# Kernel optimization log

Measured on AMD Instinct MI355X. Metric: run time of the kernel, lower is better.

## Reference

```python
import jax, jax.numpy as jnp
import numpy as np

SEQ_LEN = 2048
EMBED = 1024
HIDDEN = 1024
BATCH = 4


def setup_inputs() -> dict:
    key = jax.random.key(0)
    ks = jax.random.split(key, 7)
    # xavier_uniform for weights: limit = sqrt(6/(fan_in+fan_out))
    lim = float(np.sqrt(6.0 / (EMBED + HIDDEN)))
    blim = float(1.0 / np.sqrt(EMBED))  # torch Linear default bias init U(-1/sqrt(fan_in), ...)
    inputs = jax.random.normal(ks[0], (BATCH, SEQ_LEN, EMBED), dtype=jnp.float32)
    Wq = jax.random.uniform(ks[1], (HIDDEN, EMBED), jnp.float32, -lim, lim)
    Wk = jax.random.uniform(ks[2], (HIDDEN, EMBED), jnp.float32, -lim, lim)
    Wv = jax.random.uniform(ks[3], (HIDDEN, EMBED), jnp.float32, -lim, lim)
    bq = jax.random.uniform(ks[4], (HIDDEN,), jnp.float32, -blim, blim)
    bk = jax.random.uniform(ks[5], (HIDDEN,), jnp.float32, -blim, blim)
    bv = jax.random.uniform(ks[6], (HIDDEN,), jnp.float32, -blim, blim)
    return {"inputs": inputs, "Wq": Wq, "bq": bq, "Wk": Wk, "bk": bk, "Wv": Wv, "bv": bv}


def reference(inputs, Wq, bq, Wk, bk, Wv, bv):
    B, S, E = inputs.shape
    q = jnp.einsum('bse,he->bsh', inputs, Wq) + bq  # [B,S,H]
    k = jnp.einsum('bse,he->bsh', inputs, Wk) + bk
    v = jnp.einsum('bse,he->bsh', inputs, Wv) + bv
    # NOTE: source scales by 1/sqrt(embed_size), not hidden_size
    scores = jnp.einsum('bqh,bkh->bqk', q, k) / jnp.sqrt(jnp.float32(E))
    causal = jnp.tril(jnp.ones((S, S), dtype=bool))  # [S,S]
    scores = jnp.where(causal[None, :, :], scores, -jnp.inf)
    attn = jax.nn.softmax(scores, axis=-1)
    return jnp.einsum('bqk,bkh->bqh', attn, v)
```

## Files before the change

kernel.cpp:

```cpp
#include <hip/hip_runtime.h>
#include <cstdint>
#include <cstddef>
#include <math.h>

typedef unsigned short u16;

#define S_LEN 2048
#define EMB   1024
#define HID   1024
#define NB    4

using bf16x8 = __attribute__((ext_vector_type(8))) __bf16;
using f32x4  = __attribute__((ext_vector_type(4))) float;


__device__ __forceinline__ u16 f2bf(float f) {
  union { float f; uint32_t u; } c; c.f = f;
  uint32_t u = c.u;
  uint32_t r = (u + 0x7fffu + ((u >> 16) & 1u)) >> 16;
  return (u16)r;
}

__device__ __forceinline__ float bf2f(uint32_t hi16) {
  union { uint32_t u; float f; } c; c.u = hi16;
  return c.f;
}

__device__ __forceinline__ void gld_lds16(const u16* g, u16* l) {
  auto gp = (const __attribute__((address_space(1))) uint32_t*)(uintptr_t)(const void*)g;
  auto lp = (__attribute__((address_space(3))) uint32_t*)(uintptr_t)(void*)l;
  __builtin_amdgcn_global_load_lds(gp, lp, 16, 0, 0);
}


__global__ void cvt_all(const float* __restrict__ x,  const float* __restrict__ wq,
                        const float* __restrict__ wk, const float* __restrict__ wv,
                        u16* __restrict__ xb, u16* __restrict__ wb, int nx4, int nw4lg2) {
  const int nw4 = 1 << nw4lg2;
  const int total = nx4 + 3 * nw4;
  int i = blockIdx.x * blockDim.x + threadIdx.x;
  const int stride = gridDim.x * blockDim.x;
  for (; i < total; i += stride) {
    const float* src; u16* dst; int j;
    if (i < nx4) { src = x; dst = xb; j = i; }
    else {
      const int k = i - nx4;
      const int wsel = k >> nw4lg2;
      j = k & (nw4 - 1);
      src = (wsel == 0) ? wq : (wsel == 1) ? wk : wv;
      dst = wb + ((size_t)wsel << (nw4lg2 + 2));
    }
    float4 v = reinterpret_cast<const float4*>(src)[j];
    reinterpret_cast<ushort4*>(dst)[j] =
      make_ushort4(f2bf(v.x), f2bf(v.y), f2bf(v.z), f2bf(v.w));
  }
}


template<int EPI>
__global__ __launch_bounds__(256, 2)
void gemmT(const u16* __restrict__ A, const u16* __restrict__ Bw, void* __restrict__ Cv,
           const float* __restrict__ b0, const float* __restrict__ b1,
           const float* __restrict__ b2, u16* __restrict__ VT,
           int N, long sA, long sB, long sC, float scale)
{
  constexpr int K = 1024;
  constexpr int NTILE = K / 64;
  const int z = blockIdx.z;
  A  += (long)z * sA;
  Bw += (long)z * sB;

  __shared__ __align__(16) u16 smem[32768];

  const int tid = threadIdx.x;
  const int l   = tid & 63;
  const int w   = tid >> 6;
  const int wr  = w >> 1;
  const int wc  = w & 1;

  int bm, bn;
  if constexpr (EPI == 2) {
    const int x0 = blockIdx.x;
    const int x  = (x0 & 7) * ((int)gridDim.x >> 3) + (x0 >> 3);
    int bi = (int)((sqrtf(8.0f * (float)x + 1.0f) - 1.0f) * 0.5f);
    while ((bi + 1) * (bi + 2) / 2 <= x) ++bi;
    while (bi * (bi + 1) / 2 > x) --bi;
    bm = bi * 128;
    bn = (x - bi * (bi + 1) / 2) * 128;
  } else {
    const int nwg = gridDim.x * gridDim.y;
    const int lin = blockIdx.y * gridDim.x + blockIdx.x;
    const int sw  = (lin & 7) * (nwg >> 3) + (lin >> 3);
    bm = (sw / gridDim.x) * 128;
    bn = (sw % gridDim.x) * 128;
  }

  const int arow = w * 16 + (l >> 2);
  const int acs  = (l & 3) ^ (((l >> 5) & 1) << 1);
  const u16* gbA  = A  + (long)(bm + arow) * K + acs * 8;
  const u16* gbA2 = gbA + 64L * K;
  const u16* gbB  = Bw + (long)(bn + arow) * K + acs * 8;
  const u16* gbB2 = gbB + 64L * K;

#define STGH(t, s, dbase)                                                       \
  do {                                                                          \
    const long _o = (long)(t) * 64 + (s) * 32;                                  \
    gld_lds16(gbA  + _o, smem + (dbase) + (s) * 4096 +        w * 512);         \
    gld_lds16(gbA2 + _o, smem + (dbase) + (s) * 4096 + 2048 + w * 512);         \
    gld_lds16(gbB  + _o, smem + (dbase) + 8192 + (s) * 4096 +        w * 512);  \
    gld_lds16(gbB2 + _o, smem + (dbase) + 8192 + (s) * 4096 + 2048 + w * 512);  \
  } while (0)

  const int lr  = l & 15;
  const int kg  = l >> 4;
  const int kgp = kg ^ (((lr >> 3) & 1) << 1);
  int aoff[4], boff[4];
#pragma unroll
  for (int m = 0; m < 4; ++m) aoff[m] = (wr * 64 + m * 16 + lr) * 32 + kgp * 8;
#pragma unroll
  for (int n = 0; n < 4; ++n) boff[n] = (wc * 64 + n * 16 + lr) * 32 + kgp * 8;

  f32x4 acc[4][4] = {};

  STGH(0, 0, 0);
  STGH(0, 1, 0);
  asm volatile("s_waitcnt vmcnt(0)" ::: "memory");
  __builtin_amdgcn_s_barrier();
  asm volatile("" ::: "memory");

#define PHASE(d, s, STGSTMT)                                                    \
  do {                                                                          \
    const u16* hA = smem + (d) * 16384 + (s) * 4096;                            \
    const u16* hB = smem + (d) * 16384 + 8192 + (s) * 4096;                     \
    bf16x8 av[4], bv[4];                                                        \
    _Pragma("unroll")                                                           \
    for (int m_ = 0; m_ < 4; ++m_)                                              \
      av[m_] = *reinterpret_cast<const bf16x8*>(hA + aoff[m_]);                 \
    _Pragma("unroll")                                                           \
    for (int n_ = 0; n_ < 4; ++n_)                                              \
      bv[n_] = *reinterpret_cast<const bf16x8*>(hB + boff[n_]);                 \
    STGSTMT;                                                                    \
    asm volatile("s_waitcnt vmcnt(4)" ::: "memory");                            \
    __builtin_amdgcn_s_barrier();                                               \
    asm volatile("" ::: "memory");                                              \
    __builtin_amdgcn_s_setprio(1);                                              \
    _Pragma("unroll")                                                           \
    for (int m_ = 0; m_ < 4; ++m_)                                              \
      _Pragma("unroll")                                                         \
      for (int n_ = 0; n_ < 4; ++n_)                                            \
        acc[m_][n_] = __builtin_amdgcn_mfma_f32_16x16x32_bf16(                  \
            av[m_], bv[n_], acc[m_][n_], 0, 0, 0);                              \
    __builtin_amdgcn_s_setprio(0);                                              \
    asm volatile("" ::: "memory");                                              \
  } while (0)

#pragma unroll 1
  for (int i = 0; i < NTILE / 2; ++i) {
    const int t1 = 2 * i + 1;
    const int t2 = (2 * i + 2 < NTILE) ? 2 * i + 2 : NTILE - 1;
    PHASE(0, 0, STGH(t1, 0, 16384));
    PHASE(0, 1, STGH(t1, 1, 16384));
    PHASE(1, 0, STGH(t2, 0, 0));
    PHASE(1, 1, STGH(t2, 1, 0));
  }
#undef PHASE
#undef STGH

  if constexpr (EPI == 2) {
    u16* C = (u16*)Cv + (long)z * sC;
#pragma unroll
    for (int n = 0; n < 4; ++n) {
      const int col = bn + wc * 64 + n * 16 + lr;
#pragma unroll
      for (int m = 0; m < 4; ++m) {
        const int row0 = bm + wr * 64 + m * 16 + kg * 4;
#pragma unroll
        for (int q = 0; q < 4; ++q) {
          const int row = row0 + q;
          float v = acc[m][n][q] * scale;
          if (col > row) v = -1e30f;
          C[(long)row * N + col] = f2bf(v);
        }
      }
    }
  } else {
    constexpr long M = (long)NB * S_LEN;
    const int sel = bn >> 10;
    const float* bias = (sel == 0) ? b0 : (sel == 1) ? b1 : b2;
    u16* QK = (u16*)Cv;
#pragma unroll
    for (int n = 0; n < 4; ++n) {
      const int col = bn + wc * 64 + n * 16 + lr;
      const int h   = col & (HID - 1);
      const float bbv = bias[h];
#pragma unroll
      for (int m = 0; m < 4; ++m) {
        const int row0 = bm + wr * 64 + m * 16 + kg * 4;
        if (sel < 2) {
          u16* dst = QK + (long)sel * M * HID + (long)row0 * HID + h;
#pragma unroll
          for (int q = 0; q < 4; ++q)
            dst[(long)q * HID] = f2bf(acc[m][n][q] + bbv);
        } else {
          const int b = row0 >> 11;
          const int s = row0 & (S_LEN - 1);
          ushort4 o = make_ushort4(f2bf(acc[m][n][0] + bbv), f2bf(acc[m][n][1] + bbv),
                                   f2bf(acc[m][n][2] + bbv), f2bf(acc[m][n][3] + bbv));
          *reinterpret_cast<ushort4*>(VT + ((long)b * HID + h) * S_LEN + s) = o;
        }
      }
    }
  }
}


__global__ __launch_bounds__(512, 2)
void gemm_pv(const u16* __restrict__ Pm, const u16* __restrict__ VTm, float* __restrict__ Cm)
{
  const int z = blockIdx.z;
  const u16* A = Pm  + (long)z * S_LEN * S_LEN;
  const u16* B = VTm + (long)z * HID * S_LEN;
  float*    Cz = Cm  + (long)z * S_LEN * HID;

  __shared__ __align__(16) u16 smem[32768];

  const int tid = threadIdx.x;
  const int l   = tid & 63;
  const int w   = tid >> 6;
  const int wr  = w >> 2;
  const int wc  = w & 3;
  const int bn  = blockIdx.x * 128;
  const int pr  = blockIdx.y;

  const int lr  = l & 15;
  const int kg  = l >> 4;
  const int kgp = kg ^ (((lr >> 3) & 1) << 1);
  int aoff[4], boff[2];
#pragma unroll
  for (int m = 0; m < 4; ++m) aoff[m] = (wr * 64 + m * 16 + lr) * 32 + kgp * 8;
#pragma unroll
  for (int n = 0; n < 2; ++n) boff[n] = (wc * 32 + n * 16 + lr) * 32 + kgp * 8;

  const int arow = w * 16 + (l >> 2);
  const int acs  = (l & 3) ^ (((l >> 5) & 1) << 1);

#pragma unroll 1
  for (int it = 0; it < 2; ++it) {
    const int bi = (it == 0) ? (15 - pr) : pr;
    const int bm = bi * 128;
    const int NTILE = (bi + 1) * 2;

    const u16* gbA = A + (long)(bm + arow) * S_LEN + acs * 8;
    const u16* gbB = B + (long)(bn + arow) * S_LEN + acs * 8;

#define STGH(t, s, dbase)                                                       \
  do {                                                                          \
    const long _o = (long)(t) * 64 + (s) * 32;                                  \
    gld_lds16(gbA + _o, smem + (dbase) + (s) * 4096 + w * 512);                 \
    gld_lds16(gbB + _o, smem + (dbase) + 8192 + (s) * 4096 + w * 512);          \
  } while (0)

    if (it) {
      __builtin_amdgcn_s_barrier();
      asm volatile("" ::: "memory");
    }

    f32x4 acc[4][2] = {};

    STGH(0, 0, 0);
    STGH(0, 1, 0);
    asm volatile("s_waitcnt vmcnt(0)" ::: "memory");
    __builtin_amdgcn_s_barrier();
    asm volatile("" ::: "memory");

#define PHASE(d, s, STGSTMT)                                                    \
  do {                                                                          \
    const u16* hA = smem + (d) * 16384 + (s) * 4096;                            \
    const u16* hB = smem + (d) * 16384 + 8192 + (s) * 4096;                     \
    bf16x8 av[4], bv[2];                                                        \
    _Pragma("unroll")                                                           \
    for (int m_ = 0; m_ < 4; ++m_)                                              \
      av[m_] = *reinterpret_cast<const bf16x8*>(hA + aoff[m_]);                 \
    _Pragma("unroll")                                                           \
    for (int n_ = 0; n_ < 2; ++n_)                                              \
      bv[n_] = *reinterpret_cast<const bf16x8*>(hB + boff[n_]);                 \
    STGSTMT;                                                                    \
    asm volatile("s_waitcnt vmcnt(2)" ::: "memory");                            \
    __builtin_amdgcn_s_barrier();                                               \
    asm volatile("" ::: "memory");                                              \
    __builtin_amdgcn_s_setprio(1);                                              \
    _Pragma("unroll")                                                           \
    for (int m_ = 0; m_ < 4; ++m_)                                              \
      _Pragma("unroll")                                                         \
      for (int n_ = 0; n_ < 2; ++n_)                                            \
        acc[m_][n_] = __builtin_amdgcn_mfma_f32_16x16x32_bf16(                  \
            av[m_], bv[n_], acc[m_][n_], 0, 0, 0);                              \
    __builtin_amdgcn_s_setprio(0);                                              \
    asm volatile("" ::: "memory");                                              \
  } while (0)

#pragma unroll 1
    for (int i = 0; i < NTILE / 2; ++i) {
      const int t1 = 2 * i + 1;
      const int t2 = (2 * i + 2 < NTILE) ? 2 * i + 2 : NTILE - 1;
      PHASE(0, 0, STGH(t1, 0, 16384));
      PHASE(0, 1, STGH(t1, 1, 16384));
      PHASE(1, 0, STGH(t2, 0, 0));
      PHASE(1, 1, STGH(t2, 1, 0));
    }
#undef PHASE
#undef STGH

#pragma unroll
    for (int n = 0; n < 2; ++n) {
      const int col = bn + wc * 32 + n * 16 + lr;
#pragma unroll
      for (int m = 0; m < 4; ++m) {
        const int row0 = bm + wr * 64 + m * 16 + kg * 4;
#pragma unroll
        for (int q = 0; q < 4; ++q)
          Cz[(long)(row0 + q) * HID + col] = acc[m][n][q];
      }
    }
  }
}


__global__ __launch_bounds__(256)
void softmax_causal(const u16* __restrict__ Sc, u16* __restrict__ P, long sS, long sP)
{
  const int row  = blockIdx.x;
  const int z    = blockIdx.y;
  const int kend = ((row >> 7) + 1) << 7;
  const u16* srow = Sc + (long)z * sS + (long)row * S_LEN;
  u16*      prow = P  + (long)z * sP + (long)row * S_LEN;
  const int t = threadIdx.x;
  const int lane = t & 63, wave = t >> 6;

  const bool p0 = (8 * t) < kend;

  float e[8];
  float mx = -1e30f;
  if (p0) {
    uint4 u = reinterpret_cast<const uint4*>(srow)[t];
    uint32_t wv[4] = {u.x, u.y, u.z, u.w};
#pragma unroll
    for (int i = 0; i < 4; ++i) {
      const float lo = bf2f((wv[i] & 0xffffu) << 16);
      const float hi = bf2f(wv[i] & 0xffff0000u);
      e[2 * i]     = lo;
      e[2 * i + 1] = hi;
      mx = fmaxf(mx, fmaxf(lo, hi));
    }
  }

  __shared__ float red[8];
#pragma unroll
  for (int off = 32; off; off >>= 1) mx = fmaxf(mx, __shfl_down(mx, off));
  if (lane == 0) red[wave] = mx;
  __syncthreads();
  mx = fmaxf(fmaxf(red[0], red[1]), fmaxf(red[2], red[3]));

  float sm = 0.0f;
  if (p0) {
#pragma unroll
    for (int i = 0; i < 8; ++i) e[i] = __expf(e[i] - mx);
    sm = ((e[0] + e[1]) + (e[2] + e[3])) + ((e[4] + e[5]) + (e[6] + e[7]));
  }
#pragma unroll
  for (int off = 32; off; off >>= 1) sm += __shfl_down(sm, off);
  if (lane == 0) red[4 + wave] = sm;
  __syncthreads();
  sm = (red[4] + red[5]) + (red[6] + red[7]);

  const float inv = 1.0f / sm;
  if (p0) {
    uint32_t o[4];
#pragma unroll
    for (int i = 0; i < 4; ++i) {
      const uint32_t a = f2bf(e[2 * i] * inv);
      const uint32_t b = f2bf(e[2 * i + 1] * inv);
      o[i] = a | (b << 16);
    }
    reinterpret_cast<uint4*>(prow)[t] = make_uint4(o[0], o[1], o[2], o[3]);
  }
}


extern "C" void kernel_launch(void* const* d_in, const int* in_sizes, int n_in,
                              void* d_out, int out_size, void* d_ws, size_t ws_size,
                              hipStream_t stream)
{
  const float* x  = (const float*)d_in[0];
  const float* Wq = (const float*)d_in[1];
  const float* bq = (const float*)d_in[2];
  const float* Wk = (const float*)d_in[3];
  const float* bk = (const float*)d_in[4];
  const float* Wv = (const float*)d_in[5];
  const float* bv = (const float*)d_in[6];
  float* out = (float*)d_out;

  const long M = (long)NB * S_LEN;

  u16* xb  = (u16*)d_ws;
  u16* wqb = xb  + M * EMB;
  u16* Qb  = wqb + 3L * HID * EMB;
  u16* Kb  = Qb  + M * HID;
  u16* VT  = Kb  + M * HID;
  char* rest = (char*)(VT + M * HID);
  const size_t used  = (size_t)(rest - (char*)d_ws);
  const size_t ssz   = (size_t)S_LEN * S_LEN;
  const size_t need4 = used + (size_t)NB * ssz * 2 * 2;
  const int nb = (ws_size >= need4) ? NB : 1;
  u16* scores = (u16*)rest;
  u16* P      = scores + (size_t)nb * ssz;

  cvt_all<<<2048, 256, 0, stream>>>(x, Wq, Wk, Wv, xb, wqb, (int)(M * EMB / 4), 18);

  gemmT<4><<<dim3(24, 64, 1), 256, 0, stream>>>(xb, wqb, Qb, bq, bk, bv, VT,
                                                3 * HID, 0, 0, 0, 1.0f);

  const float scale = 0.03125f;
  const int TRI = 16 * 17 / 2;

  if (nb == NB) {
    dim3 gs(TRI, 1, NB);
    gemmT<2><<<gs, 256, 0, stream>>>(Qb, Kb, scores, nullptr, nullptr, nullptr, nullptr,
                                     S_LEN, (long)S_LEN * HID, (long)S_LEN * HID,
                                     (long)ssz, scale);
    softmax_causal<<<dim3(S_LEN, NB), 256, 0, stream>>>(scores, P, (long)ssz, (long)ssz);
    gemm_pv<<<dim3(8, 8, NB), 512, 0, stream>>>(P, VT, out);
  } else {
    for (int b = 0; b < NB; ++b) {
      const u16* Qbb = Qb + (long)b * S_LEN * HID;
      const u16* Kbb = Kb + (long)b * S_LEN * HID;
      const u16* VTb = VT + (long)b * HID * S_LEN;
      float* outb = out + (long)b * S_LEN * HID;
      dim3 gs(TRI, 1, 1);
      gemmT<2><<<gs, 256, 0, stream>>>(Qbb, Kbb, scores, nullptr, nullptr, nullptr, nullptr,
                                       S_LEN, 0, 0, 0, scale);
      softmax_causal<<<dim3(S_LEN, 1), 256, 0, stream>>>(scores, P, 0, 0);
      gemm_pv<<<dim3(8, 8, 1), 512, 0, stream>>>(P, VTb, outb);
    }
  }
}
```

Before: 157.9 us.

## Replace QKV projection GEMM with persistent 128x256-tile kernel using 8 waves

```diff
diff --git a/kernel.cpp b/kernel.cpp
--- a/kernel.cpp
+++ b/kernel.cpp
@@ -57,11 +57,130 @@
 }
 
 
-template<int EPI>
+__global__ __launch_bounds__(512, 1)
+void gemm_proj8(const u16* __restrict__ A, const u16* __restrict__ Bw, u16* __restrict__ QK,
+                const float* __restrict__ b0, const float* __restrict__ b1,
+                const float* __restrict__ b2, u16* __restrict__ VT)
+{
+  constexpr int K  = 1024;
+  constexpr int NH = K / 32;
+  constexpr long M = (long)NB * S_LEN;
+
+  __shared__ __align__(16) u16 smem[49152];
+
+  const int tid = threadIdx.x;
+  const int l   = tid & 63;
+  const int w   = tid >> 6;
+  const int wr  = w >> 2;
+  const int wc  = w & 3;
+
+  const int lr  = l & 15;
+  const int kg  = l >> 4;
+  const int kgp = kg ^ (((lr >> 3) & 1) << 1);
+  int aoff[4], boff[4];
+#pragma unroll
+  for (int m = 0; m < 4; ++m) aoff[m] = (wr * 64 + m * 16 + lr) * 32 + kgp * 8;
+#pragma unroll
+  for (int n = 0; n < 4; ++n) boff[n] = 4096 + (wc * 64 + n * 16 + lr) * 32 + kgp * 8;
+
+  const int srow = tid >> 2;
+  const int acs  = (tid & 3) ^ (((tid >> 5) & 1) << 1);
+
+#pragma unroll 1
+  for (int t = 0; t < 3; ++t) {
+    const int g  = blockIdx.x + t * 256;
+    const int bm = (g & 63) * 128;
+    const int bn = (g >> 6) * 256;
+
+    const u16* gbA  = A  + (long)(bm + srow) * K + acs * 8;
+    const u16* gbB  = Bw + (long)(bn + srow) * K + acs * 8;
+    const u16* gbB2 = gbB + 128L * K;
+
+#define STGH(h, rb)                                                             \
+  do {                                                                          \
+    const long _o = (long)(h) * 32;                                             \
+    gld_lds16(gbA  + _o, smem + (rb) +              w * 512);                   \
+    gld_lds16(gbB  + _o, smem + (rb) + 4096 +       w * 512);                   \
+    gld_lds16(gbB2 + _o, smem + (rb) + 4096 + 4096 + w * 512);                  \
+  } while (0)
+
+    if (t) {
+      __builtin_amdgcn_s_barrier();
+      asm volatile("" ::: "memory");
+    }
+
+    f32x4 acc[4][4] = {};
+
+    STGH(0, 0);
+    STGH(1, 12288);
+    asm volatile("s_waitcnt vmcnt(3)" ::: "memory");
+    __builtin_amdgcn_s_barrier();
+    asm volatile("" ::: "memory");
+
+#pragma unroll 1
+    for (int p = 0; p < NH; ++p) {
+      const u16* hR = smem + (p & 3) * 12288;
+
+      bf16x8 av[4], bv[4];
+#pragma unroll
+      for (int m_ = 0; m_ < 4; ++m_)
+        av[m_] = *reinterpret_cast<const bf16x8*>(hR + aoff[m_]);
+#pragma unroll
+      for (int n_ = 0; n_ < 4; ++n_)
+        bv[n_] = *reinterpret_cast<const bf16x8*>(hR + boff[n_]);
+
+      if (p + 2 < NH) {
+        const int rb = ((p + 2) & 3) * 12288;
+        STGH(p + 2, rb);
+        asm volatile("s_waitcnt vmcnt(3)" ::: "memory");
+      } else {
+        asm volatile("s_waitcnt vmcnt(0)" ::: "memory");
+      }
+      __builtin_amdgcn_s_barrier();
+      asm volatile("" ::: "memory");
+
+      __builtin_amdgcn_s_setprio(1);
+#pragma unroll
+      for (int m_ = 0; m_ < 4; ++m_)
+#pragma unroll
+        for (int n_ = 0; n_ < 4; ++n_)
+          acc[m_][n_] = __builtin_amdgcn_mfma_f32_16x16x32_bf16(
+              av[m_], bv[n_], acc[m_][n_], 0, 0, 0);
+      __builtin_amdgcn_s_setprio(0);
+      asm volatile("" ::: "memory");
+    }
+#undef STGH
+
+    const int sel = (bn + wc * 64) >> 10;
+    const float* bias = (sel == 0) ? b0 : (sel == 1) ? b1 : b2;
+#pragma unroll
+    for (int n = 0; n < 4; ++n) {
+      const int col = bn + wc * 64 + n * 16 + lr;
+      const int h   = col & (HID - 1);
+      const float bbv = bias[h];
+#pragma unroll
+      for (int m = 0; m < 4; ++m) {
+        const int row0 = bm + wr * 64 + m * 16 + kg * 4;
+        if (sel < 2) {
+          u16* dst = QK + (long)sel * M * HID + (long)row0 * HID + h;
+#pragma unroll
+          for (int q = 0; q < 4; ++q)
+            dst[(long)q * HID] = f2bf(acc[m][n][q] + bbv);
+        } else {
+          const int b = row0 >> 11;
+          const int s = row0 & (S_LEN - 1);
+          ushort4 o = make_ushort4(f2bf(acc[m][n][0] + bbv), f2bf(acc[m][n][1] + bbv),
+                                   f2bf(acc[m][n][2] + bbv), f2bf(acc[m][n][3] + bbv));
+          *reinterpret_cast<ushort4*>(VT + ((long)b * HID + h) * S_LEN + s) = o;
+        }
+      }
+    }
+  }
+}
+
+
 __global__ __launch_bounds__(256, 2)
 void gemmT(const u16* __restrict__ A, const u16* __restrict__ Bw, void* __restrict__ Cv,
-           const float* __restrict__ b0, const float* __restrict__ b1,
-           const float* __restrict__ b2, u16* __restrict__ VT,
            int N, long sA, long sB, long sC, float scale)
 {
   constexpr int K = 1024;
@@ -78,22 +197,13 @@
   const int wr  = w >> 1;
   const int wc  = w & 1;
 
-  int bm, bn;
-  if constexpr (EPI == 2) {
-    const int x0 = blockIdx.x;
-    const int x  = (x0 & 7) * ((int)gridDim.x >> 3) + (x0 >> 3);
-    int bi = (int)((sqrtf(8.0f * (float)x + 1.0f) - 1.0f) * 0.5f);
-    while ((bi + 1) * (bi + 2) / 2 <= x) ++bi;
-    while (bi * (bi + 1) / 2 > x) --bi;
-    bm = bi * 128;
-    bn = (x - bi * (bi + 1) / 2) * 128;
-  } else {
-    const int nwg = gridDim.x * gridDim.y;
-    const int lin = blockIdx.y * gridDim.x + blockIdx.x;
-    const int sw  = (lin & 7) * (nwg >> 3) + (lin >> 3);
-    bm = (sw / gridDim.x) * 128;
-    bn = (sw % gridDim.x) * 128;
-  }
+  const int x0 = blockIdx.x;
+  const int x  = (x0 & 7) * ((int)gridDim.x >> 3) + (x0 >> 3);
+  int bi = (int)((sqrtf(8.0f * (float)x + 1.0f) - 1.0f) * 0.5f);
+  while ((bi + 1) * (bi + 2) / 2 <= x) ++bi;
+  while (bi * (bi + 1) / 2 > x) --bi;
+  const int bm = bi * 128;
+  const int bn = (x - bi * (bi + 1) / 2) * 128;
 
   const int arow = w * 16 + (l >> 2);
   const int acs  = (l & 3) ^ (((l >> 5) & 1) << 1);
@@ -166,48 +276,19 @@
 #undef PHASE
 #undef STGH
 
-  if constexpr (EPI == 2) {
-    u16* C = (u16*)Cv + (long)z * sC;
-#pragma unroll
-    for (int n = 0; n < 4; ++n) {
-      const int col = bn + wc * 64 + n * 16 + lr;
-#pragma unroll
-      for (int m = 0; m < 4; ++m) {
-        const int row0 = bm + wr * 64 + m * 16 + kg * 4;
-#pragma unroll
-        for (int q = 0; q < 4; ++q) {
-          const int row = row0 + q;
-          float v = acc[m][n][q] * scale;
-          if (col > row) v = -1e30f;
-          C[(long)row * N + col] = f2bf(v);
-        }
-      }
-    }
-  } else {
-    constexpr long M = (long)NB * S_LEN;
-    const int sel = bn >> 10;
-    const float* bias = (sel == 0) ? b0 : (sel == 1) ? b1 : b2;
-    u16* QK = (u16*)Cv;
-#pragma unroll
-    for (int n = 0; n < 4; ++n) {
-      const int col = bn + wc * 64 + n * 16 + lr;
-      const int h   = col & (HID - 1);
-      const float bbv = bias[h];
-#pragma unroll
-      for (int m = 0; m < 4; ++m) {
-        const int row0 = bm + wr * 64 + m * 16 + kg * 4;
-        if (sel < 2) {
-          u16* dst = QK + (long)sel * M * HID + (long)row0 * HID + h;
-#pragma unroll
-          for (int q = 0; q < 4; ++q)
-            dst[(long)q * HID] = f2bf(acc[m][n][q] + bbv);
-        } else {
-          const int b = row0 >> 11;
-          const int s = row0 & (S_LEN - 1);
-          ushort4 o = make_ushort4(f2bf(acc[m][n][0] + bbv), f2bf(acc[m][n][1] + bbv),
-                                   f2bf(acc[m][n][2] + bbv), f2bf(acc[m][n][3] + bbv));
-          *reinterpret_cast<ushort4*>(VT + ((long)b * HID + h) * S_LEN + s) = o;
-        }
+  u16* C = (u16*)Cv + (long)z * sC;
+#pragma unroll
+  for (int n = 0; n < 4; ++n) {
+    const int col = bn + wc * 64 + n * 16 + lr;
+#pragma unroll
+    for (int m = 0; m < 4; ++m) {
+      const int row0 = bm + wr * 64 + m * 16 + kg * 4;
+#pragma unroll
+      for (int q = 0; q < 4; ++q) {
+        const int row = row0 + q;
+        float v = acc[m][n][q] * scale;
+        if (col > row) v = -1e30f;
+        C[(long)row * N + col] = f2bf(v);
       }
     }
   }
@@ -417,17 +498,16 @@
 
   cvt_all<<<2048, 256, 0, stream>>>(x, Wq, Wk, Wv, xb, wqb, (int)(M * EMB / 4), 18);
 
-  gemmT<4><<<dim3(24, 64, 1), 256, 0, stream>>>(xb, wqb, Qb, bq, bk, bv, VT,
-                                                3 * HID, 0, 0, 0, 1.0f);
+  gemm_proj8<<<256, 512, 0, stream>>>(xb, wqb, Qb, bq, bk, bv, VT);
 
   const float scale = 0.03125f;
   const int TRI = 16 * 17 / 2;
 
   if (nb == NB) {
     dim3 gs(TRI, 1, NB);
-    gemmT<2><<<gs, 256, 0, stream>>>(Qb, Kb, scores, nullptr, nullptr, nullptr, nullptr,
-                                     S_LEN, (long)S_LEN * HID, (long)S_LEN * HID,
-                                     (long)ssz, scale);
+    gemmT<<<gs, 256, 0, stream>>>(Qb, Kb, scores,
+                                  S_LEN, (long)S_LEN * HID, (long)S_LEN * HID,
+                                  (long)ssz, scale);
     softmax_causal<<<dim3(S_LEN, NB), 256, 0, stream>>>(scores, P, (long)ssz, (long)ssz);
     gemm_pv<<<dim3(8, 8, NB), 512, 0, stream>>>(P, VT, out);
   } else {
@@ -437,8 +517,7 @@
       const u16* VTb = VT + (long)b * HID * S_LEN;
       float* outb = out + (long)b * S_LEN * HID;
       dim3 gs(TRI, 1, 1);
-      gemmT<2><<<gs, 256, 0, stream>>>(Qbb, Kbb, scores, nullptr, nullptr, nullptr, nullptr,
-                                       S_LEN, 0, 0, 0, scale);
+      gemmT<<<gs, 256, 0, stream>>>(Qbb, Kbb, scores, S_LEN, 0, 0, 0, scale);
       softmax_causal<<<dim3(S_LEN, 1), 256, 0, stream>>>(scores, P, 0, 0);
       gemm_pv<<<dim3(8, 8, 1), 512, 0, stream>>>(P, VTb, outb);
     }
```

Result: no change. 155.8 us (-1.3%).
